# Kernel tuning notes

Measured on AMD Instinct MI355X. Metric: run time of the kernel, lower is better.

## Reference

```python
import jax, jax.numpy as jnp
import numpy as np

B, L, C, Q, H = 32, 2048, 512, 512, 1024

def setup_inputs() -> dict:
    key = jax.random.key(0)
    ks = jax.random.split(key, 8)
    query = jax.random.normal(ks[0], (B, Q), dtype=jnp.float32)
    context = jax.random.normal(ks[1], (B, L, C), dtype=jnp.float32)
    mapping_mask = jax.random.randint(ks[2], (B, L, 1), 0, 2).astype(jnp.float32)
    s = 0.02
    Wq = jax.random.normal(ks[3], (H, Q), dtype=jnp.float32) * s
    Wc = jax.random.normal(ks[4], (H, C), dtype=jnp.float32) * s
    bc = jnp.zeros((H,), dtype=jnp.float32)
    Wo = jax.random.normal(ks[5], (1, H), dtype=jnp.float32) * s
    bo = jnp.zeros((1,), dtype=jnp.float32)
    return {"query": query, "context": context, "mapping_mask": mapping_mask,
            "Wq": Wq, "Wc": Wc, "bc": bc, "Wo": Wo, "bo": bo}

def reference(query, context, mapping_mask, Wq, Wc, bc, Wo, bo):
    # res_q: [B,H], res_c: [B,L,H]
    res_q = query @ Wq.T
    res_c = jnp.einsum('blc,hc->blh', context, Wc) + bc
    tmp = jnp.tanh(res_q[:, None, :] + res_c)            # [B,L,H]
    weights_logit = jnp.einsum('blh,oh->blo', tmp, Wo) + bo  # [B,L,1]
    weights_exp = mapping_mask * jnp.exp(weights_logit)      # unnormalized, no max-subtract (faithful)
    weights = weights_exp / (weights_exp.sum(axis=1, keepdims=True) + 1e-5)
    output = jnp.einsum('blo,blc->boc', weights, context)[:, 0, :]  # bmm(w^T, ctx) -> squeeze
    return output, weights
```

## Files before the change

### kernel.cpp

```cpp
#include <hip/hip_runtime.h>

#define NB 32
#define LL 2048
#define CH 512
#define BQ 512
#define HH 1024
#define LDA 520

typedef __attribute__((ext_vector_type(8))) short bf16x8;
typedef __attribute__((ext_vector_type(16))) float f32x16;

__device__ __forceinline__ unsigned short f2bf(float x) {
  unsigned int u = __float_as_uint(x);
  u += 0x7FFFu + ((u >> 16) & 1u);
  return (unsigned short)(u >> 16);
}

__device__ __forceinline__ float fast_tanh(float x) {
  float e = __expf(2.0f * x);
  return 1.0f - 2.0f * __builtin_amdgcn_rcpf(e + 1.0f);
}

__global__ __launch_bounds__(256) void k_resqc(const float* __restrict__ query,
                                               const float* __restrict__ Wq,
                                               const float* __restrict__ bc,
                                               float* __restrict__ resqc) {
  int gid = blockIdx.x * 256 + threadIdx.x;
  int b = gid >> 10, h = gid & 1023;
  const float4* q4 = (const float4*)(query + (size_t)b * BQ);
  const float4* w4 = (const float4*)(Wq + (size_t)h * BQ);
  float acc = 0.f;
#pragma unroll 4
  for (int i = 0; i < BQ / 4; ++i) {
    float4 a = q4[i], w = w4[i];
    acc += a.x * w.x + a.y * w.y + a.z * w.z + a.w * w.w;
  }
  resqc[gid] = acc + bc[h];
}

__global__ __launch_bounds__(256) void k_pack_wc(const float* __restrict__ Wc,
                                                 unsigned short* __restrict__ wcbp) {
  int gid = blockIdx.x * 256 + threadIdx.x;
  int lane = gid & 63, ks = (gid >> 6) & 31, cg = gid >> 11;
  int lo = lane & 31, hi = lane >> 5;
  const float4* s = (const float4*)(Wc + (size_t)(cg * 32 + lo) * CH + hi * 8 + ks * 16);
  float4 v0 = s[0], v1 = s[1];
  union { unsigned short s[8]; uint4 u; } p;
  p.s[0] = f2bf(v0.x); p.s[1] = f2bf(v0.y); p.s[2] = f2bf(v0.z); p.s[3] = f2bf(v0.w);
  p.s[4] = f2bf(v1.x); p.s[5] = f2bf(v1.y); p.s[6] = f2bf(v1.z); p.s[7] = f2bf(v1.w);
  ((uint4*)wcbp)[gid] = p.u;
}

__global__ __launch_bounds__(512, 4) void k_logits(const float* __restrict__ ctx,
                                                   const unsigned short* __restrict__ wcbp,
                                                   const float* __restrict__ resqc,
                                                   const float* __restrict__ Wo,
                                                   float* __restrict__ part) {
  __shared__ unsigned short Alds[64 * LDA];
  __shared__ float lsum[64];

  int t = threadIdx.x;
  int bid = blockIdx.x;
  int swz = (bid & 7) * 256 + (bid >> 3);
  int lt = swz >> 1, hh = swz & 1;
  int b = lt >> 5;
  int row0 = (lt & 31) << 6;

  if (t < 64) lsum[t] = 0.f;

  const float4* src = (const float4*)(ctx + ((size_t)(b * LL + row0)) * CH);
#pragma unroll
  for (int p = 0; p < 16; ++p) {
    int f = p * 512 + t;
    int r = f >> 7, c4 = f & 127;
    float4 v = src[f];
    union { unsigned short s[4]; uint2 u; } pk;
    pk.s[0] = f2bf(v.x); pk.s[1] = f2bf(v.y); pk.s[2] = f2bf(v.z); pk.s[3] = f2bf(v.w);
    *(uint2*)(Alds + r * LDA + c4 * 4) = pk.u;
  }
  __syncthreads();

  int wave = t >> 6, lane = t & 63;
  int lo = lane & 31, hi = lane >> 5;

  const char* a0b = (const char*)Alds + lo * (LDA * 2) + hi * 16;
  const char* a1b = a0b + 32 * (LDA * 2);

  int n0 = hh * 512 + wave * 64;
  int cg0 = n0 >> 5;
  const uint4* bp0 = (const uint4*)wcbp + (size_t)(cg0 * 32) * 64 + lane;
  const uint4* bp1 = (const uint4*)wcbp + (size_t)((cg0 + 1) * 32) * 64 + lane;

  f32x16 acc00 = {0,0,0,0,0,0,0,0,0,0,0,0,0,0,0,0};
  f32x16 acc01 = {0,0,0,0,0,0,0,0,0,0,0,0,0,0,0,0};
  f32x16 acc10 = {0,0,0,0,0,0,0,0,0,0,0,0,0,0,0,0};
  f32x16 acc11 = {0,0,0,0,0,0,0,0,0,0,0,0,0,0,0,0};

#pragma unroll 8
  for (int ks = 0; ks < 32; ++ks) {
    uint4 ub0 = bp0[ks * 64];
    uint4 ub1 = bp1[ks * 64];
    bf16x8 fa0 = *(const bf16x8*)(a0b + ks * 32);
    bf16x8 fa1 = *(const bf16x8*)(a1b + ks * 32);
    bf16x8 fb0, fb1;
    __builtin_memcpy(&fb0, &ub0, 16);
    __builtin_memcpy(&fb1, &ub1, 16);
    acc00 = __builtin_amdgcn_mfma_f32_32x32x16_bf16(fa0, fb0, acc00, 0, 0, 0);
    acc01 = __builtin_amdgcn_mfma_f32_32x32x16_bf16(fa0, fb1, acc01, 0, 0, 0);
    acc10 = __builtin_amdgcn_mfma_f32_32x32x16_bf16(fa1, fb0, acc10, 0, 0, 0);
    acc11 = __builtin_amdgcn_mfma_f32_32x32x16_bf16(fa1, fb1, acc11, 0, 0, 0);
  }

  float qA = resqc[b * HH + n0 + lo], qB = resqc[b * HH + n0 + 32 + lo];
  float wA = Wo[n0 + lo],             wB = Wo[n0 + 32 + lo];
  float p0[16], p1[16];
#pragma unroll
  for (int r = 0; r < 16; ++r) {
    p0[r] = wA * fast_tanh(acc00[r] + qA) + wB * fast_tanh(acc01[r] + qB);
    p1[r] = wA * fast_tanh(acc10[r] + qA) + wB * fast_tanh(acc11[r] + qB);
  }
#pragma unroll
  for (int m = 16; m >= 1; m >>= 1) {
#pragma unroll
    for (int r = 0; r < 16; ++r) {
      p0[r] += __shfl_xor(p0[r], m, 64);
      p1[r] += __shfl_xor(p1[r], m, 64);
    }
  }
  if (lo == 0) {
#pragma unroll
    for (int r = 0; r < 16; ++r) {
      int row_a = (r & 3) + 8 * (r >> 2) + 4 * hi;
      atomicAdd(&lsum[row_a], p0[r]);
      atomicAdd(&lsum[32 + row_a], p1[r]);
    }
  }
  __syncthreads();
  if (t < 64) part[(size_t)hh * NB * LL + (size_t)b * LL + row0 + t] = lsum[t];
}

__global__ __launch_bounds__(256) void k_weights(const float* __restrict__ mask,
                                                 const float* __restrict__ bo,
                                                 const float* __restrict__ part,
                                                 float* __restrict__ wout) {
  __shared__ float red[4];
  int b = blockIdx.x, t = threadIdx.x;
  float bov = bo[0];
  float w[8];
  float s = 0.f;
#pragma unroll
  for (int i = 0; i < 8; ++i) {
    int l = t + 256 * i;
    float lg = part[b * LL + l] + part[NB * LL + b * LL + l] + bov;
    float e = mask[b * LL + l] * __expf(lg);
    w[i] = e; s += e;
  }
#pragma unroll
  for (int m = 32; m >= 1; m >>= 1) s += __shfl_xor(s, m, 64);
  int wave = t >> 6, lane = t & 63;
  if (lane == 0) red[wave] = s;
  __syncthreads();
  float inv = 1.0f / (red[0] + red[1] + red[2] + red[3] + 1e-5f);
#pragma unroll
  for (int i = 0; i < 8; ++i) wout[b * LL + t + 256 * i] = w[i] * inv;
}

__global__ __launch_bounds__(256) void k_output(const float* __restrict__ ctx,
                                                const float* __restrict__ weights,
                                                float* __restrict__ out) {
  __shared__ float wl[128];
  int bid = blockIdx.x;
  int b = bid >> 4, chunk = bid & 15;
  int t = threadIdx.x;
  int l0 = chunk * 128;
  if (t < 128) wl[t] = weights[b * LL + l0 + t];
  __syncthreads();
  const float2* c2 = (const float2*)(ctx + ((size_t)(b * LL + l0)) * CH) + t;
  float ax = 0.f, ay = 0.f;
#pragma unroll 4
  for (int l = 0; l < 128; ++l) {
    float wv = wl[l];
    float2 v = c2[(size_t)l * (CH / 2)];
    ax += wv * v.x; ay += wv * v.y;
  }
  atomicAdd(&out[b * CH + 2 * t], ax);
  atomicAdd(&out[b * CH + 2 * t + 1], ay);
}

extern "C" void kernel_launch(void* const* d_in, const int* in_sizes, int n_in,
                              void* d_out, int out_size, void* d_ws, size_t ws_size,
                              hipStream_t stream) {
  const float* query = (const float*)d_in[0];
  const float* ctx   = (const float*)d_in[1];
  const float* mask  = (const float*)d_in[2];
  const float* Wq    = (const float*)d_in[3];
  const float* Wc    = (const float*)d_in[4];
  const float* bc    = (const float*)d_in[5];
  const float* Wo    = (const float*)d_in[6];
  const float* bo    = (const float*)d_in[7];
  float* out = (float*)d_out;

  unsigned short* wcbp = (unsigned short*)d_ws;
  float* resqc = (float*)((char*)d_ws + (1 << 20));
  float* part  = (float*)((char*)d_ws + (1 << 20) + (1 << 17));
  float* wout = out + NB * CH;

  hipMemsetAsync(out, 0, NB * CH * sizeof(float), stream);
  k_resqc<<<128, 256, 0, stream>>>(query, Wq, bc, resqc);
  k_pack_wc<<<256, 256, 0, stream>>>(Wc, wcbp);
  k_logits<<<2048, 512, 0, stream>>>(ctx, wcbp, resqc, Wo, part);
  k_weights<<<32, 256, 0, stream>>>(mask, bo, part, wout);
  k_output<<<512, 256, 0, stream>>>(ctx, wout, out);
}
```

Before: 144.6 us.

## Make logits kernel persistent over four tiles with double-buffered LDS prefetch

The logits kernel now runs 256 blocks of 1024 threads. Each block covers all 1024 hidden units for four consecutive 64-row tiles, so the two-half partial logits buffer and the sum in the weights kernel go away. The next tile's context is loaded into registers during the current tile's epilogue and stored into a second LDS buffer, overlapping global loads with tanh and reduction work. It also adds a packed bf16 convert instruction, an exp2-based tanh, and a transpose-style shuffle reduction that replaces many shuffles and LDS atomics. The cost is fewer blocks (256 on a large GPU), high register pressure with 1024 threads, and double the LDS footprint, which may hurt occupancy.

```diff
diff --git a/kernel.cpp b/kernel.cpp
--- a/kernel.cpp
+++ b/kernel.cpp
@@ -16,8 +16,14 @@
   return (unsigned short)(u >> 16);
 }
 
+__device__ __forceinline__ unsigned int cvt_pk_bf16(float a, float b) {
+  unsigned int r;
+  asm("v_cvt_pk_bf16_f32 %0, %1, %2" : "=v"(r) : "v"(a), "v"(b));
+  return r;
+}
+
 __device__ __forceinline__ float fast_tanh(float x) {
-  float e = __expf(2.0f * x);
+  float e = __builtin_amdgcn_exp2f(x * 2.885390081777927f);
   return 1.0f - 2.0f * __builtin_amdgcn_rcpf(e + 1.0f);
 }
 
@@ -51,97 +57,118 @@
   ((uint4*)wcbp)[gid] = p.u;
 }
 
-__global__ __launch_bounds__(512, 4) void k_logits(const float* __restrict__ ctx,
-                                                   const unsigned short* __restrict__ wcbp,
-                                                   const float* __restrict__ resqc,
-                                                   const float* __restrict__ Wo,
-                                                   float* __restrict__ part) {
-  __shared__ unsigned short Alds[64 * LDA];
-  __shared__ float lsum[64];
-
-  int t = threadIdx.x;
-  int bid = blockIdx.x;
-  int swz = (bid & 7) * 256 + (bid >> 3);
-  int lt = swz >> 1, hh = swz & 1;
-  int b = lt >> 5;
-  int row0 = (lt & 31) << 6;
-
-  if (t < 64) lsum[t] = 0.f;
-
-  const float4* src = (const float4*)(ctx + ((size_t)(b * LL + row0)) * CH);
-#pragma unroll
-  for (int p = 0; p < 16; ++p) {
-    int f = p * 512 + t;
-    int r = f >> 7, c4 = f & 127;
-    float4 v = src[f];
-    union { unsigned short s[4]; uint2 u; } pk;
-    pk.s[0] = f2bf(v.x); pk.s[1] = f2bf(v.y); pk.s[2] = f2bf(v.z); pk.s[3] = f2bf(v.w);
-    *(uint2*)(Alds + r * LDA + c4 * 4) = pk.u;
+__global__ __launch_bounds__(1024, 4) void k_logits(const float* __restrict__ ctx,
+                                                    const unsigned short* __restrict__ wcbp,
+                                                    const float* __restrict__ resqc,
+                                                    const float* __restrict__ Wo,
+                                                    float* __restrict__ logits) {
+  __shared__ unsigned short Alds[2][64 * LDA];
+  __shared__ float lsum4[4][64];
+
+  const int t = threadIdx.x;
+  const int bid = blockIdx.x;
+  const int g0 = bid * 4;
+
+  if (t < 256) lsum4[t >> 6][t & 63] = 0.f;
+
+  {
+    int b = g0 >> 5, row0 = (g0 & 31) << 6;
+    const float4* src = (const float4*)(ctx + ((size_t)(b * LL + row0)) * CH);
+#pragma unroll
+    for (int i = 0; i < 8; ++i) {
+      int f = i * 1024 + t;
+      int r = f >> 7, c4 = f & 127;
+      float4 v = src[f];
+      uint2 w;
+      w.x = cvt_pk_bf16(v.x, v.y);
+      w.y = cvt_pk_bf16(v.z, v.w);
+      *(uint2*)(Alds[0] + r * LDA + c4 * 4) = w;
+    }
   }
   __syncthreads();
 
-  int wave = t >> 6, lane = t & 63;
-  int lo = lane & 31, hi = lane >> 5;
-
-  const char* a0b = (const char*)Alds + lo * (LDA * 2) + hi * 16;
-  const char* a1b = a0b + 32 * (LDA * 2);
-
-  int n0 = hh * 512 + wave * 64;
-  int cg0 = n0 >> 5;
-  const uint4* bp0 = (const uint4*)wcbp + (size_t)(cg0 * 32) * 64 + lane;
-  const uint4* bp1 = (const uint4*)wcbp + (size_t)((cg0 + 1) * 32) * 64 + lane;
-
-  f32x16 acc00 = {0,0,0,0,0,0,0,0,0,0,0,0,0,0,0,0};
-  f32x16 acc01 = {0,0,0,0,0,0,0,0,0,0,0,0,0,0,0,0};
-  f32x16 acc10 = {0,0,0,0,0,0,0,0,0,0,0,0,0,0,0,0};
-  f32x16 acc11 = {0,0,0,0,0,0,0,0,0,0,0,0,0,0,0,0};
-
+  const int wave = t >> 6, lane = t & 63;
+  const int lo = lane & 31, hi = lane >> 5;
+  const int n0 = wave * 64;
+  const uint4* bp0 = (const uint4*)wcbp + (size_t)(wave * 2) * 32 * 64 + lane;
+  const uint4* bp1 = bp0 + 32 * 64;
+  const float wA = Wo[n0 + lo], wB = Wo[n0 + 32 + lo];
+
+  for (int tt = 0; tt < 4; ++tt) {
+    const int g = g0 + tt;
+    const int b = g >> 5, row0 = (g & 31) << 6;
+    const int cur = tt & 1;
+    const char* a0b = (const char*)(Alds[cur]) + lo * (LDA * 2) + hi * 16;
+    const char* a1b = a0b + 32 * (LDA * 2);
+
+    f32x16 acc00 = {0,0,0,0,0,0,0,0,0,0,0,0,0,0,0,0};
+    f32x16 acc01 = {0,0,0,0,0,0,0,0,0,0,0,0,0,0,0,0};
+    f32x16 acc10 = {0,0,0,0,0,0,0,0,0,0,0,0,0,0,0,0};
+    f32x16 acc11 = {0,0,0,0,0,0,0,0,0,0,0,0,0,0,0,0};
 #pragma unroll 8
-  for (int ks = 0; ks < 32; ++ks) {
-    uint4 ub0 = bp0[ks * 64];
-    uint4 ub1 = bp1[ks * 64];
-    bf16x8 fa0 = *(const bf16x8*)(a0b + ks * 32);
-    bf16x8 fa1 = *(const bf16x8*)(a1b + ks * 32);
-    bf16x8 fb0, fb1;
-    __builtin_memcpy(&fb0, &ub0, 16);
-    __builtin_memcpy(&fb1, &ub1, 16);
-    acc00 = __builtin_amdgcn_mfma_f32_32x32x16_bf16(fa0, fb0, acc00, 0, 0, 0);
-    acc01 = __builtin_amdgcn_mfma_f32_32x32x16_bf16(fa0, fb1, acc01, 0, 0, 0);
-    acc10 = __builtin_amdgcn_mfma_f32_32x32x16_bf16(fa1, fb0, acc10, 0, 0, 0);
-    acc11 = __builtin_amdgcn_mfma_f32_32x32x16_bf16(fa1, fb1, acc11, 0, 0, 0);
-  }
-
-  float qA = resqc[b * HH + n0 + lo], qB = resqc[b * HH + n0 + 32 + lo];
-  float wA = Wo[n0 + lo],             wB = Wo[n0 + 32 + lo];
-  float p0[16], p1[16];
-#pragma unroll
-  for (int r = 0; r < 16; ++r) {
-    p0[r] = wA * fast_tanh(acc00[r] + qA) + wB * fast_tanh(acc01[r] + qB);
-    p1[r] = wA * fast_tanh(acc10[r] + qA) + wB * fast_tanh(acc11[r] + qB);
-  }
-#pragma unroll
-  for (int m = 16; m >= 1; m >>= 1) {
+    for (int ks = 0; ks < 32; ++ks) {
+      uint4 ub0 = bp0[ks * 64];
+      uint4 ub1 = bp1[ks * 64];
+      bf16x8 fa0 = *(const bf16x8*)(a0b + ks * 32);
+      bf16x8 fa1 = *(const bf16x8*)(a1b + ks * 32);
+      bf16x8 fb0, fb1;
+      __builtin_memcpy(&fb0, &ub0, 16);
+      __builtin_memcpy(&fb1, &ub1, 16);
+      acc00 = __builtin_amdgcn_mfma_f32_32x32x16_bf16(fa0, fb0, acc00, 0, 0, 0);
+      acc01 = __builtin_amdgcn_mfma_f32_32x32x16_bf16(fa0, fb1, acc01, 0, 0, 0);
+      acc10 = __builtin_amdgcn_mfma_f32_32x32x16_bf16(fa1, fb0, acc10, 0, 0, 0);
+      acc11 = __builtin_amdgcn_mfma_f32_32x32x16_bf16(fa1, fb1, acc11, 0, 0, 0);
+    }
+
+    float4 sv[8];
+    if (tt < 3) {
+      int gn = g + 1;
+      int nb = gn >> 5, nrow0 = (gn & 31) << 6;
+      const float4* srcn = (const float4*)(ctx + ((size_t)(nb * LL + nrow0)) * CH);
+#pragma unroll
+      for (int i = 0; i < 8; ++i) sv[i] = srcn[i * 1024 + t];
+    }
+
+    float qA = resqc[b * HH + n0 + lo], qB = resqc[b * HH + n0 + 32 + lo];
+    float v[32];
 #pragma unroll
     for (int r = 0; r < 16; ++r) {
-      p0[r] += __shfl_xor(p0[r], m, 64);
-      p1[r] += __shfl_xor(p1[r], m, 64);
-    }
-  }
-  if (lo == 0) {
-#pragma unroll
-    for (int r = 0; r < 16; ++r) {
-      int row_a = (r & 3) + 8 * (r >> 2) + 4 * hi;
-      atomicAdd(&lsum[row_a], p0[r]);
-      atomicAdd(&lsum[32 + row_a], p1[r]);
-    }
-  }
-  __syncthreads();
-  if (t < 64) part[(size_t)hh * NB * LL + (size_t)b * LL + row0 + t] = lsum[t];
+      v[r]      = wA * fast_tanh(acc00[r] + qA) + wB * fast_tanh(acc01[r] + qB);
+      v[16 + r] = wA * fast_tanh(acc10[r] + qA) + wB * fast_tanh(acc11[r] + qB);
+    }
+#pragma unroll
+    for (int s = 16; s >= 1; s >>= 1) {
+#pragma unroll
+      for (int i = 0; i < s; ++i) {
+        float a = v[i], c = v[i + s];
+        float keep = (lo & s) ? c : a;
+        float send = (lo & s) ? a : c;
+        v[i] = keep + __shfl_xor(send, s, 64);
+      }
+    }
+    int rr = lo & 15;
+    int row = ((lo < 16) ? 0 : 32) + (rr & 3) + 8 * (rr >> 2) + 4 * hi;
+    atomicAdd(&lsum4[tt][row], v[0]);
+
+    if (tt < 3) {
+#pragma unroll
+      for (int i = 0; i < 8; ++i) {
+        int f = i * 1024 + t;
+        int r = f >> 7, c4 = f & 127;
+        uint2 w;
+        w.x = cvt_pk_bf16(sv[i].x, sv[i].y);
+        w.y = cvt_pk_bf16(sv[i].z, sv[i].w);
+        *(uint2*)(Alds[cur ^ 1] + r * LDA + c4 * 4) = w;
+      }
+    }
+    __syncthreads();
+    if (t < 64) logits[(size_t)b * LL + row0 + t] = lsum4[tt][t];
+  }
 }
 
 __global__ __launch_bounds__(256) void k_weights(const float* __restrict__ mask,
                                                  const float* __restrict__ bo,
-                                                 const float* __restrict__ part,
+                                                 const float* __restrict__ logit,
                                                  float* __restrict__ wout) {
   __shared__ float red[4];
   int b = blockIdx.x, t = threadIdx.x;
@@ -151,8 +178,7 @@
 #pragma unroll
   for (int i = 0; i < 8; ++i) {
     int l = t + 256 * i;
-    float lg = part[b * LL + l] + part[NB * LL + b * LL + l] + bov;
-    float e = mask[b * LL + l] * __expf(lg);
+    float e = mask[b * LL + l] * __expf(logit[b * LL + l] + bov);
     w[i] = e; s += e;
   }
 #pragma unroll
@@ -202,13 +228,13 @@
 
   unsigned short* wcbp = (unsigned short*)d_ws;
   float* resqc = (float*)((char*)d_ws + (1 << 20));
-  float* part  = (float*)((char*)d_ws + (1 << 20) + (1 << 17));
+  float* logit = (float*)((char*)d_ws + (1 << 20) + (1 << 17));
   float* wout = out + NB * CH;
 
   hipMemsetAsync(out, 0, NB * CH * sizeof(float), stream);
   k_resqc<<<128, 256, 0, stream>>>(query, Wq, bc, resqc);
   k_pack_wc<<<256, 256, 0, stream>>>(Wc, wcbp);
-  k_logits<<<2048, 512, 0, stream>>>(ctx, wcbp, resqc, Wo, part);
-  k_weights<<<32, 256, 0, stream>>>(mask, bo, part, wout);
+  k_logits<<<256, 1024, 0, stream>>>(ctx, wcbp, resqc, Wo, logit);
+  k_weights<<<32, 256, 0, stream>>>(mask, bo, logit, wout);
   k_output<<<512, 256, 0, stream>>>(ctx, wout, out);
 }
```

Result: slower. 171.3 us (+18.5%).
